# Performance work log

Measured on AMD Instinct MI355X. Metric: run time of the kernel, lower is better.

The kernel has to match this reference:

```python
import jax, jax.numpy as jnp
import numpy as np
import math

D = 256
NH = 4
MULT = 128
N = MULT * D // NH  # 8192
N_LAYER = 6
VOCAB = 256
THETA = 2 ** 16
EPS = 1e-5


def get_freqs(n):
    ar = jnp.arange(n, dtype=jnp.float32)
    q = jnp.floor(ar / 2.0) * 2.0  # quantize in pairs
    return 1.0 / (THETA ** (q / n)) / (2.0 * math.pi)


def layer_norm(x):
    m = jnp.mean(x, axis=-1, keepdims=True)
    v = jnp.var(x, axis=-1, keepdims=True)
    return (x - m) / jnp.sqrt(v + EPS)


def rope_apply(v, cos, sin):
    # interleaved rotation: v_rot = stack((-v[odd], v[even])) interleaved back
    v_rot = jnp.stack([-v[..., 1::2], v[..., ::2]], axis=-1).reshape(v.shape)
    return v * cos + v_rot * sin


def setup_inputs() -> dict:
    key = jax.random.key(0)
    ks = jax.random.split(key, 6)
    idx = jax.random.randint(ks[0], (1, 1024), 0, VOCAB)
    embed = jax.random.normal(ks[1], (VOCAB, D), dtype=jnp.float32) * 0.02
    encoder = jax.random.normal(ks[2], (NH, D, N), dtype=jnp.float32) * 0.02
    encoder_v = jax.random.normal(ks[3], (NH, D, N), dtype=jnp.float32) * 0.02
    decoder = jax.random.normal(ks[4], (NH * N, D), dtype=jnp.float32) * 0.02
    lm_head = jax.random.normal(ks[5], (D, VOCAB), dtype=jnp.float32) * 0.02
    return {"idx": idx, "embed": embed, "encoder": encoder,
            "encoder_v": encoder_v, "decoder": decoder, "lm_head": lm_head}


def reference(idx, embed, encoder, encoder_v, decoder, lm_head):
    B, T = idx.shape
    x = layer_norm(embed[idx])  # (B, T, D)

    freqs = get_freqs(N)  # (N,)
    phases = (jnp.arange(T, dtype=jnp.float32)[:, None] * freqs[None, :]) % 1.0
    phases = phases * (2.0 * math.pi)
    cos = jnp.cos(phases)[None, None]  # (1,1,T,N)
    sin = jnp.sin(phases)[None, None]

    causal = jnp.tril(jnp.ones((T, T), dtype=jnp.float32), k=-1)  # strict lower

    for _ in range(N_LAYER):
        # x_sparse: (B, nh, T, N)
        x_sparse = jax.nn.relu(jnp.einsum('btd,hdn->bhtn', x, encoder))
        QR = rope_apply(x_sparse, cos, sin)
        # raw (no-softmax) strictly-causal attention, V = x broadcast over heads
        scores = jnp.einsum('bhtn,bhsn->bhts', QR, QR) * causal
        yKV = layer_norm(jnp.einsum('bhts,bsd->bhtd', scores, x))
        y_sparse = jax.nn.relu(jnp.einsum('bhtd,hdn->bhtn', yKV, encoder_v))
        xy = x_sparse * y_sparse  # (B, nh, T, N)
        # head-major flatten then project back to D
        yMLP = xy.transpose(0, 2, 1, 3).reshape(B, T, NH * N) @ decoder
        y = layer_norm(yMLP)
        x = layer_norm(x + y)

    logits = x @ lm_head  # (B, T, VOCAB)
    return logits
```

## Files before the change

kernel.cpp:

```cpp
#include <hip/hip_runtime.h>
#include <math.h>


typedef __bf16 bf16;
typedef bf16  bf16x2 __attribute__((ext_vector_type(2)));
typedef bf16  bf16x8 __attribute__((ext_vector_type(8)));
typedef float f32x4  __attribute__((ext_vector_type(4)));

#define BM 128
#define BN 128
#define BK 32
#define SW 32

typedef __attribute__((address_space(3))) unsigned int lds_uint;
typedef const __attribute__((address_space(1))) unsigned int glb_uint;

__device__ __forceinline__ void ld_g2l16(const void* g, void* l) {
  __builtin_amdgcn_global_load_lds((glb_uint*)g, (lds_uint*)l, 16, 0, 0);
}

__device__ __forceinline__ float block_sum256(float v) {
  __shared__ float sb[4];
#pragma unroll
  for (int o = 32; o > 0; o >>= 1) v += __shfl_down(v, o);
  __syncthreads();
  if ((threadIdx.x & 63) == 0) sb[threadIdx.x >> 6] = v;
  __syncthreads();
  return sb[0] + sb[1] + sb[2] + sb[3];
}

template <int MODE>
__global__ __launch_bounds__(256) void gemm_bt(
    const bf16* __restrict__ A, long lda, long aZ, long aZ2,
    const bf16* __restrict__ Bt, long ldb, long bZ, long bZ2,
    void* __restrict__ Cv, long ldc, long cZ,
    void* __restrict__ Dv, long dZ,
    int M, int N, int K) {
  int m0, n0;
  long z = blockIdx.z;
  if (MODE == 6) {
    const int combo = blockIdx.x;
    const int tile  = blockIdx.y;
    const int tr = (int)((sqrtf(8.f * tile + 1.f) - 1.f) * 0.5f);
    const int tc = tile - tr * (tr + 1) / 2;
    m0 = tr * BM; n0 = tc * BN;
    A  += (long)(combo >> 3) * aZ2 + (long)(combo & 7) * aZ;
    Bt += (long)(combo >> 3) * bZ2 + (long)(combo & 7) * bZ;
  } else if (MODE == 7) {
    const int combo = blockIdx.x;
    z = combo;
    m0 = (blockIdx.y >> 1) * BM;
    n0 = (blockIdx.y & 1) * BN;
    A  += (combo & 7) * aZ + (combo >> 3) * aZ2;
    Bt += (combo & 7) * bZ + (combo >> 3) * bZ2;
  } else {
    m0 = blockIdx.y * BM;
    n0 = blockIdx.x * BN;
    if (MODE == 2 && n0 > m0) return;
    A  += (z & 3) * aZ + (z >> 2) * aZ2;
    Bt += (z & 3) * bZ + (z >> 2) * bZ2;
  }

  __shared__ __align__(16) bf16 As[3][BM * SW];
  __shared__ __align__(16) bf16 Bs[3][BN * SW];

  const int tid  = threadIdx.x;
  const int lane = tid & 63;
  const int wr   = (tid >> 6) >> 1;
  const int wc   = (tid >> 6) & 1;
  const int l15  = lane & 15;
  const int qd   = lane >> 4;

  f32x4 acc[4][4] = {};

  int Keff = K;
  if (MODE == 3) { int kc = m0 + BM; Keff = kc < K ? kc : K; }

  const int srow = tid >> 2;
  const int skc  = (tid & 3) * 8;
  const bf16* ap = A + (long)(m0 + srow) * lda + skc;
  const bf16* bp = Bt + (long)(n0 + srow) * ldb + skc;

  auto stage = [&](int buf, int k0) {
    char* AsB = (char*)&As[buf][0];
    char* BsB = (char*)&Bs[buf][0];
    ld_g2l16(ap + k0,            AsB + tid * 16);
    ld_g2l16(ap + k0 + 64 * lda, AsB + 4096 + tid * 16);
    ld_g2l16(bp + k0,            BsB + tid * 16);
    ld_g2l16(bp + k0 + 64 * ldb, BsB + 4096 + tid * 16);
  };
  auto compute = [&](int buf) {
    bf16x8 af[4], bfr[4];
#pragma unroll
    for (int i = 0; i < 4; i++)
      af[i] = *(const bf16x8*)&As[buf][(wr * 64 + i * 16 + l15) * SW + qd * 8];
#pragma unroll
    for (int j = 0; j < 4; j++)
      bfr[j] = *(const bf16x8*)&Bs[buf][(wc * 64 + j * 16 + l15) * SW + qd * 8];
#pragma unroll
    for (int i = 0; i < 4; i++)
#pragma unroll
      for (int j = 0; j < 4; j++)
        acc[i][j] = __builtin_amdgcn_mfma_f32_16x16x32_bf16(af[i], bfr[j], acc[i][j], 0, 0, 0);
  };

  const int nst = Keff >> 5;
  stage(0, 0);
  stage(1, BK);
  int bc = 0;
  for (int k = 0; k < nst - 1; k++) {
    asm volatile("s_waitcnt vmcnt(4)" ::: "memory");
    __builtin_amdgcn_s_barrier();
    const int k2 = k + 2;
    if (k2 < nst) {
      int b2 = bc + 2; if (b2 >= 3) b2 -= 3;
      stage(b2, k2 * BK);
    }
    compute(bc);
    bc = (bc + 1 == 3) ? 0 : bc + 1;
  }
  asm volatile("s_waitcnt vmcnt(0)" ::: "memory");
  __builtin_amdgcn_s_barrier();
  compute(bc);

#pragma unroll
  for (int i = 0; i < 4; i++) {
#pragma unroll
    for (int j = 0; j < 4; j++) {
#pragma unroll
      for (int r = 0; r < 4; r++) {
        const int row = m0 + wr * 64 + i * 16 + qd * 4 + r;
        const int col = n0 + wc * 64 + j * 16 + l15;
        float v = acc[i][j][r];
        if (MODE == 1) {
          float rv = fmaxf(v, 0.f);
          float pv = __shfl_xor(rv, 1);
          ((bf16*)Cv)[z * cZ + (long)row * ldc + col] = (bf16)rv;
          float freq = exp2f(-(float)(col >> 1) * (1.0f / 256.0f)) * 0.15915494309189535f;
          float ph = (float)row * freq;
          ph -= floorf(ph);
          float s, c;
          __sincosf(ph * 6.283185307179586f, &s, &c);
          float rot = (col & 1) ? pv : -pv;
          ((bf16*)Dv)[z * dZ + (long)row * ldc + col] = (bf16)(rv * c + rot * s);
        } else if (MODE == 2) {
          ((bf16*)Cv)[z * cZ + (long)row * ldc + col] = (bf16)((col < row) ? v : 0.f);
        } else if (MODE == 4) {
          float rv = fmaxf(v, 0.f);
          float xv = (float)((const bf16*)Dv)[z * dZ + (long)row * 8192 + col];
          ((bf16*)Cv)[z * cZ + (long)row * ldc + col] = (bf16)(rv * xv);
        } else if (MODE == 6) {
          const int combo = blockIdx.x;
          long base = (((long)(combo & 7) * 4 + (combo >> 3)) * 36 + blockIdx.y) * 16384;
          ((bf16*)Cv)[base + (long)(row - m0) * 128 + (col - n0)] = (bf16)v;
        } else {
          ((float*)Cv)[z * cZ + (long)row * ldc + col] = v;
        }
      }
    }
  }
}

__global__ void reduce_sc(const bf16* __restrict__ scpart, bf16* __restrict__ sc) {
  const int tile = blockIdx.x >> 2, q = blockIdx.x & 3, head = blockIdx.y;
  const int tr = (int)((sqrtf(8.f * tile + 1.f) - 1.f) * 0.5f);
  const int tc = tile - tr * (tr + 1) / 2;
  const long t0p = ((long)head * 589824 + (long)tile * 16384) >> 1;
  const bf16x2* sp = (const bf16x2*)scpart;
  for (int p = q * 2048 + threadIdx.x; p < q * 2048 + 2048; p += 256) {
    float s0 = 0.f, s1 = 0.f;
#pragma unroll
    for (int s = 0; s < 8; s++) {
      bf16x2 v = sp[(long)s * 1179648 + t0p + p];
      s0 += (float)v.x; s1 += (float)v.y;
    }
    int i = p * 2;
    int lr = i >> 7, lc = i & 127;
    int grow = tr * 128 + lr, gcol = tc * 128 + lc;
    bf16x2 o;
    o.x = (bf16)((gcol < grow) ? s0 : 0.f);
    o.y = (bf16)((gcol + 1 < grow) ? s1 : 0.f);
    *(bf16x2*)&sc[(long)head * 1048576 + (long)grow * 1024 + gcol] = o;
  }
}

__global__ void transpose_cvt(const float* __restrict__ in, bf16* __restrict__ out,
                              int R, int C, long inZ, long outZ) {
  in += (long)blockIdx.z * inZ;
  out += (long)blockIdx.z * outZ;
  __shared__ float tile[32][33];
  int c0 = blockIdx.x * 32, r0 = blockIdx.y * 32;
  int lc = threadIdx.x & 31, lr8 = threadIdx.x >> 5;
#pragma unroll
  for (int i = 0; i < 32; i += 8)
    tile[lr8 + i][lc] = in[(long)(r0 + lr8 + i) * C + c0 + lc];
  __syncthreads();
#pragma unroll
  for (int i = 0; i < 32; i += 8)
    out[(long)(c0 + lr8 + i) * R + r0 + lc] = (bf16)tile[lc][lr8 + i];
}

__global__ void embed_ln(const int* __restrict__ idx, const float* __restrict__ embed,
                         float* __restrict__ x, bf16* __restrict__ xb,
                         bf16* __restrict__ xT) {
  int t = blockIdx.x, d = threadIdx.x;
  float v = embed[(long)idx[t] * 256 + d];
  float m = block_sum256(v) * (1.0f / 256.0f);
  float c = v - m;
  float var = block_sum256(c * c) * (1.0f / 256.0f);
  float o = c * rsqrtf(var + 1e-5f);
  x[t * 256 + d] = o;
  xb[t * 256 + d] = (bf16)o;
  xT[d * 1024 + t] = (bf16)o;
}

__global__ void ln_rows(const float* __restrict__ in, bf16* __restrict__ out) {
  int r = blockIdx.x, d = threadIdx.x;
  float v = in[(long)r * 256 + d];
  float m = block_sum256(v) * (1.0f / 256.0f);
  float c = v - m;
  float var = block_sum256(c * c) * (1.0f / 256.0f);
  out[(long)r * 256 + d] = (bf16)(c * rsqrtf(var + 1e-5f));
}

__global__ void ln_fuse(const float* __restrict__ part, float* __restrict__ x,
                        bf16* __restrict__ xb, bf16* __restrict__ xT) {
  int t = blockIdx.x, d = threadIdx.x;
  float s = 0.f;
#pragma unroll
  for (int i = 0; i < 32; i++) s += part[(long)i * 262144 + t * 256 + d];
  float m = block_sum256(s) * (1.0f / 256.0f);
  float c = s - m;
  float var = block_sum256(c * c) * (1.0f / 256.0f);
  float y = c * rsqrtf(var + 1e-5f);
  float zv = x[t * 256 + d] + y;
  m = block_sum256(zv) * (1.0f / 256.0f);
  c = zv - m;
  var = block_sum256(c * c) * (1.0f / 256.0f);
  float o = c * rsqrtf(var + 1e-5f);
  x[t * 256 + d] = o;
  xb[t * 256 + d] = (bf16)o;
  xT[d * 1024 + t] = (bf16)o;
}

extern "C" void kernel_launch(void* const* d_in, const int* in_sizes, int n_in,
                              void* d_out, int out_size, void* d_ws, size_t ws_size,
                              hipStream_t stream) {
  const int*   idx = (const int*)d_in[0];
  const float* emb = (const float*)d_in[1];
  float* out = (float*)d_out;
  char* ws  = (char*)d_ws;

  bf16*  encT   = (bf16*)(ws + 0L);
  bf16*  encvT  = (bf16*)(ws + 16777216L);
  bf16*  decT   = (bf16*)(ws + 33554432L);
  bf16*  lmT    = (bf16*)(ws + 50331648L);
  float* x      = (float*)(ws + 50462720L);
  bf16*  xb     = (bf16*)(ws + 51511296L);
  bf16*  xT     = (bf16*)(ws + 52035584L);
  bf16*  xs     = (bf16*)(ws + 52559872L);
  bf16*  qr     = (bf16*)(ws + 119668736L);
  bf16*  sc     = (bf16*)(ws + 186777600L);
  bf16*  scpart = (bf16*)(ws + 195166208L);
  float* ykv    = (float*)(ws + 195166208L);
  bf16*  ykvln  = (bf16*)(ws + 199360512L);
  float* part   = (float*)(ws + 195166208L);
  const bool big = ws_size >= 232914944UL;

  transpose_cvt<<<dim3(256, 8, 4), dim3(256), 0, stream>>>((const float*)d_in[2], encT, 256, 8192, 2097152L, 2097152L);
  transpose_cvt<<<dim3(256, 8, 4), dim3(256), 0, stream>>>((const float*)d_in[3], encvT, 256, 8192, 2097152L, 2097152L);
  transpose_cvt<<<dim3(8, 1024, 1), dim3(256), 0, stream>>>((const float*)d_in[4], decT, 32768, 256, 0L, 0L);
  transpose_cvt<<<dim3(8, 8, 1), dim3(256), 0, stream>>>((const float*)d_in[5], lmT, 256, 256, 0L, 0L);
  embed_ln<<<dim3(1024), dim3(256), 0, stream>>>(idx, emb, x, xb, xT);

  for (int l = 0; l < 6; l++) {
    gemm_bt<1><<<dim3(64, 8, 4), dim3(256), 0, stream>>>(
        xb, 256L, 0L, 0L, encT, 256L, 2097152L, 8388608L,
        (void*)xs, 8192L, 8388608L, (void*)qr, 8388608L, 1024, 8192, 256);
    if (big) {
      gemm_bt<6><<<dim3(32, 36), dim3(256), 0, stream>>>(
          qr, 8192L, 1024L, 8388608L, qr, 8192L, 1024L, 8388608L,
          (void*)scpart, 0L, 0L, (void*)0, 0L, 1024, 1024, 1024);
      reduce_sc<<<dim3(144, 4), dim3(256), 0, stream>>>(scpart, sc);
    } else {
      gemm_bt<2><<<dim3(8, 8, 4), dim3(256), 0, stream>>>(
          qr, 8192L, 8388608L, 33554432L, qr, 8192L, 8388608L, 33554432L,
          (void*)sc, 1024L, 1048576L, (void*)0, 0L, 1024, 1024, 8192);
    }
    gemm_bt<3><<<dim3(2, 8, 4), dim3(256), 0, stream>>>(
        sc, 1024L, 1048576L, 4194304L, xT, 1024L, 0L, 0L,
        (void*)ykv, 256L, 262144L, (void*)0, 0L, 1024, 256, 1024);
    ln_rows<<<dim3(4096), dim3(256), 0, stream>>>(ykv, ykvln);
    gemm_bt<4><<<dim3(64, 8, 4), dim3(256), 0, stream>>>(
        ykvln, 256L, 262144L, 1048576L, encvT, 256L, 2097152L, 8388608L,
        (void*)qr, 8192L, 8388608L, (void*)xs, 8388608L, 1024, 8192, 256);
    gemm_bt<7><<<dim3(32, 16), dim3(256), 0, stream>>>(
        qr, 8192L, 1024L, 8388608L, decT, 32768L, 1024L, 8192L,
        (void*)part, 256L, 262144L, (void*)0, 0L, 1024, 256, 1024);
    ln_fuse<<<dim3(1024), dim3(256), 0, stream>>>(part, x, xb, xT);
  }
  gemm_bt<5><<<dim3(2, 8, 1), dim3(256), 0, stream>>>(
      xb, 256L, 0L, 0L, lmT, 256L, 0L, 0L,
      (void*)out, 256L, 0L, (void*)0, 0L, 1024, 256, 256);
}
```

Measured before the change: 1.416 ms.

## Split-K the scores-by-x GEMM, store decoder partials as bf16, vectorize reduce_sc

The causal scores×x GEMM (mode 3) is now split along K into four 256-wide slices per head, giving 16 z-slices instead of 4. Blocks whose slice lies entirely above the causal limit exit early. ln_rows sums only the partial slices that are active for each row before the layernorm. The decoder split-K partials are written as bf16 instead of fp32, halving the traffic into ln_fuse at some cost in accuracy. reduce_sc now loads and stores 8 bf16 values per access instead of 2.

```diff
diff --git a/kernel.cpp b/kernel.cpp
--- a/kernel.cpp
+++ b/kernel.cpp
@@ -3,7 +3,6 @@
 
 
 typedef __bf16 bf16;
-typedef bf16  bf16x2 __attribute__((ext_vector_type(2)));
 typedef bf16  bf16x8 __attribute__((ext_vector_type(8)));
 typedef float f32x4  __attribute__((ext_vector_type(4)));
 
@@ -61,6 +60,16 @@
     Bt += (z & 3) * bZ + (z >> 2) * bZ2;
   }
 
+  int kbeg = 0;
+  int Keff = K;
+  if (MODE == 3) {
+    const int s = (int)(z & 3);
+    kbeg = s * 256;
+    const int kc = m0 + BM;
+    Keff = (kbeg + 256 < kc) ? kbeg + 256 : kc;
+    if (kbeg >= Keff) return;
+  }
+
   __shared__ __align__(16) bf16 As[3][BM * SW];
   __shared__ __align__(16) bf16 Bs[3][BN * SW];
 
@@ -72,9 +81,6 @@
   const int qd   = lane >> 4;
 
   f32x4 acc[4][4] = {};
-
-  int Keff = K;
-  if (MODE == 3) { int kc = m0 + BM; Keff = kc < K ? kc : K; }
 
   const int srow = tid >> 2;
   const int skc  = (tid & 3) * 8;
@@ -104,9 +110,9 @@
         acc[i][j] = __builtin_amdgcn_mfma_f32_16x16x32_bf16(af[i], bfr[j], acc[i][j], 0, 0, 0);
   };
 
-  const int nst = Keff >> 5;
-  stage(0, 0);
-  stage(1, BK);
+  const int nst = (Keff - kbeg) >> 5;
+  stage(0, kbeg);
+  stage(1, kbeg + BK);
   int bc = 0;
   for (int k = 0; k < nst - 1; k++) {
     asm volatile("s_waitcnt vmcnt(4)" ::: "memory");
@@ -114,7 +120,7 @@
     const int k2 = k + 2;
     if (k2 < nst) {
       int b2 = bc + 2; if (b2 >= 3) b2 -= 3;
-      stage(b2, k2 * BK);
+      stage(b2, kbeg + k2 * BK);
     }
     compute(bc);
     bc = (bc + 1 == 3) ? 0 : bc + 1;
@@ -153,6 +159,8 @@
           const int combo = blockIdx.x;
           long base = (((long)(combo & 7) * 4 + (combo >> 3)) * 36 + blockIdx.y) * 16384;
           ((bf16*)Cv)[base + (long)(row - m0) * 128 + (col - n0)] = (bf16)v;
+        } else if (MODE == 7) {
+          ((bf16*)Cv)[z * cZ + (long)row * ldc + col] = (bf16)v;
         } else {
           ((float*)Cv)[z * cZ + (long)row * ldc + col] = v;
         }
@@ -165,22 +173,22 @@
   const int tile = blockIdx.x >> 2, q = blockIdx.x & 3, head = blockIdx.y;
   const int tr = (int)((sqrtf(8.f * tile + 1.f) - 1.f) * 0.5f);
   const int tc = tile - tr * (tr + 1) / 2;
-  const long t0p = ((long)head * 589824 + (long)tile * 16384) >> 1;
-  const bf16x2* sp = (const bf16x2*)scpart;
-  for (int p = q * 2048 + threadIdx.x; p < q * 2048 + 2048; p += 256) {
-    float s0 = 0.f, s1 = 0.f;
-#pragma unroll
-    for (int s = 0; s < 8; s++) {
-      bf16x2 v = sp[(long)s * 1179648 + t0p + p];
-      s0 += (float)v.x; s1 += (float)v.y;
+  const long t0 = (long)head * 589824 + (long)tile * 16384;
+  for (int g = q * 512 + threadIdx.x; g < q * 512 + 512; g += 256) {
+    const int i = g * 8;
+    float s[8] = {};
+#pragma unroll
+    for (int sl = 0; sl < 8; sl++) {
+      bf16x8 v = *(const bf16x8*)&scpart[(long)sl * 2359296 + t0 + i];
+#pragma unroll
+      for (int e = 0; e < 8; e++) s[e] += (float)v[e];
     }
-    int i = p * 2;
-    int lr = i >> 7, lc = i & 127;
-    int grow = tr * 128 + lr, gcol = tc * 128 + lc;
-    bf16x2 o;
-    o.x = (bf16)((gcol < grow) ? s0 : 0.f);
-    o.y = (bf16)((gcol + 1 < grow) ? s1 : 0.f);
-    *(bf16x2*)&sc[(long)head * 1048576 + (long)grow * 1024 + gcol] = o;
+    const int lr = i >> 7, lc = i & 127;
+    const int grow = tr * 128 + lr, gcol = tc * 128 + lc;
+    bf16x8 o;
+#pragma unroll
+    for (int e = 0; e < 8; e++) o[e] = (bf16)((gcol + e < grow) ? s[e] : 0.f);
+    *(bf16x8*)&sc[(long)head * 1048576 + (long)grow * 1024 + gcol] = o;
   }
 }
 
@@ -214,21 +222,25 @@
   xT[d * 1024 + t] = (bf16)o;
 }
 
-__global__ void ln_rows(const float* __restrict__ in, bf16* __restrict__ out) {
+__global__ void ln_rows(const float* __restrict__ ykvp, bf16* __restrict__ out) {
   int r = blockIdx.x, d = threadIdx.x;
-  float v = in[(long)r * 256 + d];
+  int h = r >> 10, t = r & 1023;
+  int ns = (t >> 8) + 1;
+  float v = 0.f;
+  for (int s = 0; s < ns; s++)
+    v += ykvp[((long)(h * 4 + s)) * 262144 + (long)t * 256 + d];
   float m = block_sum256(v) * (1.0f / 256.0f);
   float c = v - m;
   float var = block_sum256(c * c) * (1.0f / 256.0f);
   out[(long)r * 256 + d] = (bf16)(c * rsqrtf(var + 1e-5f));
 }
 
-__global__ void ln_fuse(const float* __restrict__ part, float* __restrict__ x,
+__global__ void ln_fuse(const bf16* __restrict__ part, float* __restrict__ x,
                         bf16* __restrict__ xb, bf16* __restrict__ xT) {
   int t = blockIdx.x, d = threadIdx.x;
   float s = 0.f;
 #pragma unroll
-  for (int i = 0; i < 32; i++) s += part[(long)i * 262144 + t * 256 + d];
+  for (int i = 0; i < 32; i++) s += (float)part[(long)i * 262144 + t * 256 + d];
   float m = block_sum256(s) * (1.0f / 256.0f);
   float c = s - m;
   float var = block_sum256(c * c) * (1.0f / 256.0f);
@@ -262,9 +274,9 @@
   bf16*  qr     = (bf16*)(ws + 119668736L);
   bf16*  sc     = (bf16*)(ws + 186777600L);
   bf16*  scpart = (bf16*)(ws + 195166208L);
-  float* ykv    = (float*)(ws + 195166208L);
-  bf16*  ykvln  = (bf16*)(ws + 199360512L);
-  float* part   = (float*)(ws + 195166208L);
+  float* ykvp   = (float*)(ws + 195166208L);
+  bf16*  part   = (bf16*)(ws + 195166208L);
+  bf16*  ykvln  = (bf16*)(ws + 211943424L);
   const bool big = ws_size >= 232914944UL;
 
   transpose_cvt<<<dim3(256, 8, 4), dim3(256), 0, stream>>>((const float*)d_in[2], encT, 256, 8192, 2097152L, 2097152L);
@@ -287,10 +299,10 @@
           qr, 8192L, 8388608L, 33554432L, qr, 8192L, 8388608L, 33554432L,
           (void*)sc, 1024L, 1048576L, (void*)0, 0L, 1024, 1024, 8192);
     }
-    gemm_bt<3><<<dim3(2, 8, 4), dim3(256), 0, stream>>>(
-        sc, 1024L, 1048576L, 4194304L, xT, 1024L, 0L, 0L,
-        (void*)ykv, 256L, 262144L, (void*)0, 0L, 1024, 256, 1024);
-    ln_rows<<<dim3(4096), dim3(256), 0, stream>>>(ykv, ykvln);
+    gemm_bt<3><<<dim3(2, 8, 16), dim3(256), 0, stream>>>(
+        sc, 1024L, 0L, 1048576L, xT, 1024L, 0L, 0L,
+        (void*)ykvp, 256L, 262144L, (void*)0, 0L, 1024, 256, 1024);
+    ln_rows<<<dim3(4096), dim3(256), 0, stream>>>(ykvp, ykvln);
     gemm_bt<4><<<dim3(64, 8, 4), dim3(256), 0, stream>>>(
         ykvln, 256L, 262144L, 1048576L, encvT, 256L, 2097152L, 8388608L,
         (void*)qr, 8192L, 8388608L, (void*)xs, 8388608L, 1024, 8192, 256);
```

Result: faster. 1.332 ms (-5.9%).
